# Kernel optimization log

Measured on AMD Instinct MI355X. Metric: run time of the kernel, lower is better.

## Reference

```python
import jax, jax.numpy as jnp
import numpy as np

B, T, L, D, H = 8, 4, 512, 512, 8
HD = D // H
THR = 1.0
BETA = 0.5
EPS = 1e-5


def heaviside(x):
    return (x >= 0).astype(x.dtype)


def bn_eval(x, g, b, rm, rv):
    # BatchNorm1d in eval mode applied on the last dim
    return (x - rm) * (g * jax.lax.rsqrt(rv + EPS)) + b


def lif(x_btld):
    # snntorch Leaky(beta=0.5, threshold=1, reset='subtract'), mem init 0, scan over T
    xs = jnp.moveaxis(x_btld, 1, 0)  # (T,B,L,D)

    def step(mem, xt):
        reset = heaviside(mem - THR)          # reset from previous mem (detached in torch)
        mem = BETA * mem + xt - reset * THR
        spk = heaviside(mem - THR)
        return mem, spk

    _, spks = jax.lax.scan(step, jnp.zeros_like(xs[0]), xs)
    return jnp.moveaxis(spks, 0, 1)


def setup_inputs() -> dict:
    key = jax.random.key(0)
    ks = jax.random.split(key, 24)
    s = D ** -0.5
    inp = {
        "x": jax.random.normal(ks[0], (B, T, L, D), jnp.float32),
        "q_w": jax.random.normal(ks[1], (D, D), jnp.float32) * s,
        "q_g": jax.random.normal(ks[2], (D,), jnp.float32),
        "q_b": jax.random.normal(ks[3], (D,), jnp.float32),
        "q_rm": jax.random.normal(ks[4], (D,), jnp.float32),
        "q_rv": jax.random.uniform(ks[5], (D,), jnp.float32),
        "k_w": jax.random.normal(ks[6], (D, D), jnp.float32) * s,
        "k_g": jax.random.normal(ks[7], (D,), jnp.float32),
        "k_b": jax.random.normal(ks[8], (D,), jnp.float32),
        "k_rm": jax.random.normal(ks[9], (D,), jnp.float32),
        "k_rv": jax.random.uniform(ks[10], (D,), jnp.float32),
        "v_w": jax.random.normal(ks[11], (D, D), jnp.float32) * s,
        "v_g": jax.random.normal(ks[12], (D,), jnp.float32),
        "v_b": jax.random.normal(ks[13], (D,), jnp.float32),
        "v_rm": jax.random.normal(ks[14], (D,), jnp.float32),
        "v_rv": jax.random.uniform(ks[15], (D,), jnp.float32),
        "o_w": jax.random.normal(ks[16], (D, D), jnp.float32) * s,
        "o_bias": jax.random.normal(ks[17], (D,), jnp.float32),
        "o_g": jax.random.normal(ks[18], (D,), jnp.float32),
        "o_b": jax.random.normal(ks[19], (D,), jnp.float32),
        "o_rm": jax.random.normal(ks[20], (D,), jnp.float32),
        "o_rv": jax.random.uniform(ks[21], (D,), jnp.float32),
    }
    return inp


def reference(x, q_w, q_g, q_b, q_rm, q_rv, k_w, k_g, k_b, k_rm, k_rv,
              v_w, v_g, v_b, v_rm, v_rv, o_w, o_bias, o_g, o_b, o_rm, o_rv):
    scale = HD ** -0.5
    # Q path: linear -> BN -> LIF (binary {0,1})
    q = bn_eval(jnp.einsum('btld,ed->btle', x, q_w), q_g, q_b, q_rm, q_rv)
    q = lif(q)
    # K path: linear -> BN -> ReLU (continuous)
    k = jax.nn.relu(bn_eval(jnp.einsum('btld,ed->btle', x, k_w), k_g, k_b, k_rm, k_rv))
    # V path: linear -> BN -> ternary {-1,0,+1}
    v = bn_eval(jnp.einsum('btld,ed->btle', x, v_w), v_g, v_b, v_rm, v_rv)
    v = heaviside(v - THR) - heaviside(-v - THR)
    # split heads: (B,T,H,L,hd)
    sh = lambda a: a.reshape(B, T, L, H, HD).transpose(0, 1, 3, 2, 4)
    q, k, v = sh(q), sh(k), sh(v)
    attn = jnp.einsum('bthld,bthmd->bthlm', q, k) * scale
    out = jnp.einsum('bthlm,bthmd->bthld', attn, v)
    out = out.transpose(0, 1, 3, 2, 4).reshape(B, T, L, D)
    out = jnp.einsum('btld,ed->btle', out, o_w) + o_bias
    out = bn_eval(out, o_g, o_b, o_rm, o_rv)
    return lif(out)
```

## Files before the change

kernel.cpp:

```cpp
#include <hip/hip_runtime.h>
#include <math.h>
#include <stdint.h>

#define Bb 8
#define Tt 4
#define Ll 512
#define Dd 512
#define Hh 8
#define HDd 64
#define Mm (Bb*Tt*Ll)

typedef _Float16 f16;
typedef _Float16 f16x8 __attribute__((ext_vector_type(8)));
typedef _Float16 f16x4 __attribute__((ext_vector_type(4)));
typedef float f32x16 __attribute__((ext_vector_type(16)));

#define LO_SCALE 2048.0f
#define LO_INV   4.8828125e-4f

__device__ __forceinline__ void gload16(const void* g, void* l) {
  __builtin_amdgcn_global_load_lds(
      (const __attribute__((address_space(1))) unsigned int*)(uintptr_t)g,
      (__attribute__((address_space(3))) unsigned int*)(uintptr_t)l,
      16, 0, 0);
}

struct SplitArgs {
  const float* src[5];
  f16* hi[5];
  f16* lo[5];
};

__global__ void split_k(SplitArgs s) {
  int i = blockIdx.x * 256 + threadIdx.x;
  int seg, base;
  if (i < 1048576) { seg = 0; base = i; }
  else { int r = i - 1048576; seg = 1 + (r >> 15); base = r & 32767; }
  const float* sp = s.src[seg] + (size_t)base * 8;
  float4 v0 = *(const float4*)sp;
  float4 v1 = *(const float4*)(sp + 4);
  float a[8] = {v0.x, v0.y, v0.z, v0.w, v1.x, v1.y, v1.z, v1.w};
  f16x8 hv, lv;
  #pragma unroll
  for (int e = 0; e < 8; ++e) {
    f16 hh = (f16)a[e];
    hv[e] = hh;
    lv[e] = (f16)((a[e] - (float)hh) * LO_SCALE);
  }
  *(f16x8*)(s.hi[seg] + (size_t)base * 8) = hv;
  *(f16x8*)(s.lo[seg] + (size_t)base * 8) = lv;
}

struct GArgs {
  const f16 *Ah, *Al;
  const f16 *Wh0, *Wl0, *Wh1, *Wl1, *Wh2, *Wl2;
  const float *g0,*b0,*rm0,*rv0;
  const float *g1,*b1,*rm1,*rv1;
  const float *g2,*b2,*rm2,*rv2;
  const float* bias;
  f16*   oq;
  float* ok;
  f16*   ov;
  float* oo;
};

#define SMEM_BYTES 34048

template<int MODE>
__global__ __launch_bounds__(256, 2)
void gemm_f16(GArgs ar) {
  extern __shared__ __align__(16) char smem[];
  f16* Ah_s = (f16*)smem;
  f16* Al_s = (f16*)(smem + 8192);
  f16* Bh_s = (f16*)(smem + 16384);
  f16* Bl_s = (f16*)(smem + 24576);
  float (*TS)[133] = (float(*)[133])smem;

  const int tid = threadIdx.x;
  const int lane = tid & 63, wid = tid >> 6;

  const int bid = blockIdx.x;
  int bx, by;
  if (MODE == 0) { const int sw = (bid & 7) * 192 + (bid >> 3); bx = sw % 12; by = sw / 12; }
  else           { const int sw = (bid & 7) * 64  + (bid >> 3); bx = sw & 3;  by = sw >> 2; }

  const int seg = (MODE == 0) ? (bx >> 2) : 0;
  const int lc0 = (MODE == 0) ? ((bx & 3) << 7) : (bx << 7);
  const int b = by >> 4, lc32 = by & 15;

  const f16* Wh = (seg == 0 ? ar.Wh0 : (seg == 1 ? ar.Wh1 : ar.Wh2));
  const f16* Wl = (seg == 0 ? ar.Wl0 : (seg == 1 ? ar.Wl1 : ar.Wl2));
  const float* gp  = (seg == 0 ? ar.g0  : (seg == 1 ? ar.g1  : ar.g2));
  const float* bp  = (seg == 0 ? ar.b0  : (seg == 1 ? ar.b1  : ar.b2));
  const float* rmp = (seg == 0 ? ar.rm0 : (seg == 1 ? ar.rm1 : ar.rm2));
  const float* rvp = (seg == 0 ? ar.rv0 : (seg == 1 ? ar.rv1 : ar.rv2));

  const int sr = lane >> 2, skc = lane & 3;
  const int skcs = skc ^ ((sr >> 1) & 3);
  const int frow = lane & 31, khalf = lane >> 5;
  const int rsw = (frow >> 1) & 3;
  const int wmr = wid >> 1, wnc = wid & 1;

  f32x16 acc_h[2][2], acc_l[2][2];
  #pragma unroll
  for (int i = 0; i < 2; ++i)
    #pragma unroll
    for (int j = 0; j < 2; ++j) {
      acc_h[i][j] = (f32x16)0.0f;
      acc_l[i][j] = (f32x16)0.0f;
    }

  for (int k0 = 0; k0 < Dd; k0 += 32) {
    __syncthreads();
    #pragma unroll
    for (int i = 0; i < 2; ++i) {
      const int r = i * 64 + wid * 16 + sr;
      const int growA = (((b << 2) + (r >> 5)) << 9) + (lc32 << 5) + (r & 31);
      const size_t goA = (size_t)growA * Dd + k0 + skcs * 8;
      const size_t goB = (size_t)(lc0 + r) * Dd + k0 + skcs * 8;
      const int lb = i * 2048 + wid * 512;
      gload16(ar.Ah + goA, Ah_s + lb);
      gload16(ar.Al + goA, Al_s + lb);
      gload16(Wh + goB, Bh_s + lb);
      gload16(Wl + goB, Bl_s + lb);
    }
    __syncthreads();

    f16x8 ah[2][2], al[2][2], bh[2][2], bl[2][2];
    #pragma unroll
    for (int mi = 0; mi < 2; ++mi) {
      const int r = wmr * 64 + mi * 32 + frow;
      #pragma unroll
      for (int ks = 0; ks < 2; ++ks) {
        const int cin = (khalf + 2 * ks) ^ rsw;
        const int ad = r * 32 + cin * 8;
        ah[mi][ks] = *(const f16x8*)&Ah_s[ad];
        al[mi][ks] = *(const f16x8*)&Al_s[ad];
      }
    }
    #pragma unroll
    for (int nj = 0; nj < 2; ++nj) {
      const int r = wnc * 64 + nj * 32 + frow;
      #pragma unroll
      for (int ks = 0; ks < 2; ++ks) {
        const int cin = (khalf + 2 * ks) ^ rsw;
        const int ad = r * 32 + cin * 8;
        bh[nj][ks] = *(const f16x8*)&Bh_s[ad];
        bl[nj][ks] = *(const f16x8*)&Bl_s[ad];
      }
    }
    #pragma unroll
    for (int ks = 0; ks < 2; ++ks)
      #pragma unroll
      for (int mi = 0; mi < 2; ++mi)
        #pragma unroll
        for (int nj = 0; nj < 2; ++nj) {
          acc_h[mi][nj] = __builtin_amdgcn_mfma_f32_32x32x16_f16(ah[mi][ks], bh[nj][ks], acc_h[mi][nj], 0, 0, 0);
          acc_l[mi][nj] = __builtin_amdgcn_mfma_f32_32x32x16_f16(ah[mi][ks], bl[nj][ks], acc_l[mi][nj], 0, 0, 0);
          acc_l[mi][nj] = __builtin_amdgcn_mfma_f32_32x32x16_f16(al[mi][ks], bh[nj][ks], acc_l[mi][nj], 0, 0, 0);
        }
  }

  float scl[2], shc[2];
  #pragma unroll
  for (int nj = 0; nj < 2; ++nj) {
    const int c = lc0 + wnc * 64 + nj * 32 + frow;
    double S = (double)gp[c] / sqrt((double)rvp[c] + 1e-5);
    double Sh = (double)bp[c] - (double)rmp[c] * S;
    if (MODE == 1) Sh += (double)ar.bias[c] * S;
    scl[nj] = (float)S; shc[nj] = (float)Sh;
  }

  if (MODE == 0 && seg != 0) {
    #pragma unroll
    for (int mi = 0; mi < 2; ++mi)
      #pragma unroll
      for (int nj = 0; nj < 2; ++nj)
        #pragma unroll
        for (int r = 0; r < 16; ++r) {
          const int row32 = (r & 3) + 8 * (r >> 2) + 4 * khalf;
          const int tr = wmr * 64 + mi * 32 + row32;
          const int grow = (((b << 2) + (tr >> 5)) << 9) + (lc32 << 5) + (tr & 31);
          const int col = lc0 + wnc * 64 + nj * 32 + frow;
          float val = acc_h[mi][nj][r] + acc_l[mi][nj][r] * LO_INV;
          float y = val * scl[nj] + shc[nj];
          if (seg == 1) ar.ok[(size_t)grow * Dd + col] = fmaxf(y, 0.f);
          else ar.ov[(size_t)grow * Dd + col] =
                   (f16)((y >= 1.f ? 1.f : 0.f) - (-y >= 1.f ? 1.f : 0.f));
        }
    return;
  }

  __syncthreads();
  #pragma unroll
  for (int half = 0; half < 2; ++half) {
    if (wnc == half) {
      #pragma unroll
      for (int mi = 0; mi < 2; ++mi)
        #pragma unroll
        for (int nj = 0; nj < 2; ++nj)
          #pragma unroll
          for (int q = 0; q < 4; ++q) {
            float4 yv;
            float* yp = &yv.x;
            #pragma unroll
            for (int rr = 0; rr < 4; ++rr) {
              const int r = q * 4 + rr;
              float val = acc_h[mi][nj][r] + acc_l[mi][nj][r] * LO_INV;
              yp[rr] = val * scl[nj] + shc[nj];
            }
            *(float4*)&TS[nj * 32 + frow][wmr * 64 + mi * 32 + 8 * q + 4 * khalf] = yv;
          }
    }
    __syncthreads();
    const int cc4 = (tid & 15) << 2;
    #pragma unroll
    for (int rr = 0; rr < 2; ++rr) {
      const int rl = (tid >> 4) + (rr << 4);
      float mm[4] = {0.f, 0.f, 0.f, 0.f};
      #pragma unroll
      for (int t = 0; t < 4; ++t) {
        const int trow = t * 32 + rl;
        float sp[4];
        #pragma unroll
        for (int c = 0; c < 4; ++c) {
          float y = TS[cc4 + c][trow];
          float rst = (mm[c] >= 1.f) ? 1.f : 0.f;
          mm[c] = 0.5f * mm[c] + y - rst;
          sp[c] = (mm[c] >= 1.f) ? 1.f : 0.f;
        }
        const size_t go = ((size_t)((((b << 2) + t) << 9) + (lc32 << 5) + rl)) * Dd
                          + lc0 + (half << 6) + cc4;
        if (MODE == 0) {
          f16x4 s4;
          s4[0] = (f16)sp[0]; s4[1] = (f16)sp[1]; s4[2] = (f16)sp[2]; s4[3] = (f16)sp[3];
          *(f16x4*)(ar.oq + go) = s4;
        } else {
          *(float4*)(ar.oo + go) = make_float4(sp[0], sp[1], sp[2], sp[3]);
        }
      }
    }
    __syncthreads();
  }
}

__global__ __launch_bounds__(256)
void attn_g(const float* __restrict__ ks, const f16* __restrict__ vs,
            float* __restrict__ pG) {
  const int bt = blockIdx.x, h = blockIdx.y, c = blockIdx.z;
  const float* kp = ks + (size_t)bt * Ll * Dd + h * HDd;
  const f16* vp = vs + (size_t)bt * Ll * Dd + h * HDd;

  __shared__ float KS[64][68];
  __shared__ float VS[64][68];
  const int tid = threadIdx.x;
  const int te = tid & 15, td = tid >> 4;

  float gacc[4][4];
  #pragma unroll
  for (int i = 0; i < 4; ++i)
    #pragma unroll
    for (int j = 0; j < 4; ++j) gacc[i][j] = 0.f;

  for (int mt = 0; mt < 2; ++mt) {
    const int m0 = c * 128 + mt * 64;
    #pragma unroll
    for (int it = 0; it < 4; ++it) {
      int fidx = it * 256 + tid;
      int row = fidx >> 4, fq = fidx & 15;
      *(float4*)&KS[row][fq << 2] = *(const float4*)(kp + (size_t)(m0 + row) * Dd + (fq << 2));
    }
    #pragma unroll
    for (int it = 0; it < 2; ++it) {
      int fidx = it * 256 + tid;
      int row = fidx >> 3, c8 = fidx & 7;
      f16x8 hv = *(const f16x8*)(vp + (size_t)(m0 + row) * Dd + (c8 << 3));
      *(float4*)&VS[row][c8 << 3] = make_float4(hv[0], hv[1], hv[2], hv[3]);
      *(float4*)&VS[row][(c8 << 3) + 4] = make_float4(hv[4], hv[5], hv[6], hv[7]);
    }
    __syncthreads();
    #pragma unroll 4
    for (int mm = 0; mm < 64; ++mm) {
      float4 k4 = *(const float4*)&KS[mm][te << 2];
      float4 v4 = *(const float4*)&VS[mm][td << 2];
      const float kk[4] = {k4.x, k4.y, k4.z, k4.w};
      const float vv[4] = {v4.x, v4.y, v4.z, v4.w};
      #pragma unroll
      for (int i = 0; i < 4; ++i)
        #pragma unroll
        for (int j = 0; j < 4; ++j)
          gacc[i][j] = fmaf(kk[i], vv[j], gacc[i][j]);
    }
    __syncthreads();
  }
  float* out = pG + (((size_t)(bt * 8 + h) * 4 + c) << 12);
  #pragma unroll
  for (int i = 0; i < 4; ++i)
    *(float4*)&out[((te << 2) + i) * 64 + (td << 2)] =
        make_float4(gacc[i][0] * 0.125f, gacc[i][1] * 0.125f,
                    gacc[i][2] * 0.125f, gacc[i][3] * 0.125f);
}

__global__ __launch_bounds__(256)
void attn_o(const f16* __restrict__ qs, const float* __restrict__ pG,
            f16* __restrict__ ahi, f16* __restrict__ alo) {
  const int bt = blockIdx.x, h = blockIdx.y, lc = blockIdx.z;
  __shared__ float G[64][68];
  __shared__ float QS[64][68];
  const int tid = threadIdx.x;

  const float* pg = pG + (((size_t)(bt * 8 + h) * 4) << 12);
  #pragma unroll
  for (int rep = 0; rep < 4; ++rep) {
    int t4 = rep * 256 + tid;
    int e = t4 >> 4, dq = t4 & 15;
    int off = e * 64 + (dq << 2);
    float4 s0 = *(const float4*)(pg + off);
    float4 s1 = *(const float4*)(pg + 4096 + off);
    float4 s2 = *(const float4*)(pg + 8192 + off);
    float4 s3 = *(const float4*)(pg + 12288 + off);
    *(float4*)&G[e][dq << 2] = make_float4(s0.x + s1.x + s2.x + s3.x,
                                           s0.y + s1.y + s2.y + s3.y,
                                           s0.z + s1.z + s2.z + s3.z,
                                           s0.w + s1.w + s2.w + s3.w);
  }
  __syncthreads();

  const f16* qp = qs + (size_t)bt * Ll * Dd + h * HDd;
  const int lr = tid >> 2, dg = tid & 3;

  for (int l0 = 0; l0 < 128; l0 += 64) {
    #pragma unroll
    for (int it = 0; it < 2; ++it) {
      int fidx = it * 256 + tid;
      int row = fidx >> 3, c8 = fidx & 7;
      f16x8 hv = *(const f16x8*)(qp + (size_t)(lc * 128 + l0 + row) * Dd + (c8 << 3));
      *(float4*)&QS[row][c8 << 3] = make_float4(hv[0], hv[1], hv[2], hv[3]);
      *(float4*)&QS[row][(c8 << 3) + 4] = make_float4(hv[4], hv[5], hv[6], hv[7]);
    }
    __syncthreads();
    float oacc[16];
    #pragma unroll
    for (int j = 0; j < 16; ++j) oacc[j] = 0.f;
    for (int ee = 0; ee < 64; ++ee) {
      float qv = QS[lr][ee];
      #pragma unroll
      for (int jq = 0; jq < 4; ++jq) {
        float4 g4 = *(const float4*)&G[ee][(dg << 4) + (jq << 2)];
        oacc[jq * 4 + 0] = fmaf(qv, g4.x, oacc[jq * 4 + 0]);
        oacc[jq * 4 + 1] = fmaf(qv, g4.y, oacc[jq * 4 + 1]);
        oacc[jq * 4 + 2] = fmaf(qv, g4.z, oacc[jq * 4 + 2]);
        oacc[jq * 4 + 3] = fmaf(qv, g4.w, oacc[jq * 4 + 3]);
      }
    }
    f16x8 h0, l0v, h1, l1v;
    #pragma unroll
    for (int t = 0; t < 8; ++t) {
      float v = oacc[t];
      f16 hh = (f16)v;
      h0[t] = hh; l0v[t] = (f16)((v - (float)hh) * LO_SCALE);
      float v2 = oacc[8 + t];
      f16 hh2 = (f16)v2;
      h1[t] = hh2; l1v[t] = (f16)((v2 - (float)hh2) * LO_SCALE);
    }
    size_t ob = ((size_t)bt * Ll + lc * 128 + l0 + lr) * Dd + h * HDd + (dg << 4);
    *(f16x8*)(ahi + ob) = h0;
    *(f16x8*)(ahi + ob + 8) = h1;
    *(f16x8*)(alo + ob) = l0v;
    *(f16x8*)(alo + ob + 8) = l1v;
    __syncthreads();
  }
}

extern "C" void kernel_launch(void* const* d_in, const int* in_sizes, int n_in,
                              void* d_out, int out_size, void* d_ws, size_t ws_size,
                              hipStream_t stream) {
  const float* x    = (const float*)d_in[0];
  const float* q_w  = (const float*)d_in[1];
  const float* q_g  = (const float*)d_in[2];
  const float* q_b  = (const float*)d_in[3];
  const float* q_rm = (const float*)d_in[4];
  const float* q_rv = (const float*)d_in[5];
  const float* k_w  = (const float*)d_in[6];
  const float* k_g  = (const float*)d_in[7];
  const float* k_b  = (const float*)d_in[8];
  const float* k_rm = (const float*)d_in[9];
  const float* k_rv = (const float*)d_in[10];
  const float* v_w  = (const float*)d_in[11];
  const float* v_g  = (const float*)d_in[12];
  const float* v_b  = (const float*)d_in[13];
  const float* v_rm = (const float*)d_in[14];
  const float* v_rv = (const float*)d_in[15];
  const float* o_w  = (const float*)d_in[16];
  const float* o_bias = (const float*)d_in[17];
  const float* o_g  = (const float*)d_in[18];
  const float* o_b  = (const float*)d_in[19];
  const float* o_rm = (const float*)d_in[20];
  const float* o_rv = (const float*)d_in[21];

  char* wsb = (char*)d_ws;
  const size_t R16 = 16777216;
  f16*   xhi  = (f16*)wsb;
  f16*   xlo  = (f16*)(wsb + R16);
  f16*   qspk = (f16*)(wsb + 2 * R16);
  float* kbuf = (float*)(wsb + 3 * R16);
  f16*   vbuf = (f16*)(wsb + 5 * R16);
  float* pG   = (float*)(wsb + 6 * R16);
  f16*   wsp  = (f16*)(wsb + 7 * R16);
  f16* qwh = wsp;            f16* qwl = wsp + 262144;
  f16* kwh = wsp + 2*262144; f16* kwl = wsp + 3*262144;
  f16* vwh = wsp + 4*262144; f16* vwl = wsp + 5*262144;
  f16* owh = wsp + 6*262144; f16* owl = wsp + 7*262144;
  f16* ahi = xhi;
  f16* alo = xlo;

  SplitArgs sa;
  sa.src[0] = x;   sa.hi[0] = xhi; sa.lo[0] = xlo;
  sa.src[1] = q_w; sa.hi[1] = qwh; sa.lo[1] = qwl;
  sa.src[2] = k_w; sa.hi[2] = kwh; sa.lo[2] = kwl;
  sa.src[3] = v_w; sa.hi[3] = vwh; sa.lo[3] = vwl;
  sa.src[4] = o_w; sa.hi[4] = owh; sa.lo[4] = owl;
  split_k<<<4608, 256, 0, stream>>>(sa);

  GArgs a1;
  a1.Ah = xhi; a1.Al = xlo;
  a1.Wh0 = qwh; a1.Wl0 = qwl; a1.Wh1 = kwh; a1.Wl1 = kwl; a1.Wh2 = vwh; a1.Wl2 = vwl;
  a1.g0 = q_g; a1.b0 = q_b; a1.rm0 = q_rm; a1.rv0 = q_rv;
  a1.g1 = k_g; a1.b1 = k_b; a1.rm1 = k_rm; a1.rv1 = k_rv;
  a1.g2 = v_g; a1.b2 = v_b; a1.rm2 = v_rm; a1.rv2 = v_rv;
  a1.bias = nullptr;
  a1.oq = qspk; a1.ok = kbuf; a1.ov = vbuf; a1.oo = nullptr;
  gemm_f16<0><<<1536, 256, SMEM_BYTES, stream>>>(a1);

  attn_g<<<dim3(32, 8, 4), 256, 0, stream>>>(kbuf, vbuf, pG);
  attn_o<<<dim3(32, 8, 4), 256, 0, stream>>>(qspk, pG, ahi, alo);

  GArgs a2;
  a2.Ah = ahi; a2.Al = alo;
  a2.Wh0 = owh; a2.Wl0 = owl; a2.Wh1 = owh; a2.Wl1 = owl; a2.Wh2 = owh; a2.Wl2 = owl;
  a2.g0 = o_g; a2.b0 = o_b; a2.rm0 = o_rm; a2.rv0 = o_rv;
  a2.g1 = o_g; a2.b1 = o_b; a2.rm1 = o_rm; a2.rv1 = o_rv;
  a2.g2 = o_g; a2.b2 = o_b; a2.rm2 = o_rm; a2.rv2 = o_rv;
  a2.bias = o_bias;
  a2.oq = nullptr; a2.ok = nullptr; a2.ov = nullptr; a2.oo = (float*)d_out;
  gemm_f16<1><<<512, 256, SMEM_BYTES, stream>>>(a2);
}
```

Baseline: 297.0 us.

## Fuse fp16 hi/lo split into GEMM tile loads and merge attention kernels

Removes the standalone split kernel. The GEMMs now load fp32 A and W tiles into shared memory with a swizzle and convert them to fp16 hi/lo pairs in registers using packed round-toward-zero conversion. The two attention kernels (partial K^T V, then Q·G) are merged into one kernel per (bt, head), and it writes fp32 output that the final GEMM consumes directly. This removes the extra global round trips for the split buffers and the partial-G reduction. In exchange, each tile is converted repeatedly by every block that reads it, the fused attention grid has a quarter as many blocks, and rounding behaviour changes because RTZ replaces round-to-nearest.

Measured after the change: 331.2 us. 1.11x slower.

```diff
diff --git a/kernel.cpp b/kernel.cpp
--- a/kernel.cpp
+++ b/kernel.cpp
@@ -13,6 +13,7 @@
 typedef _Float16 f16;
 typedef _Float16 f16x8 __attribute__((ext_vector_type(8)));
 typedef _Float16 f16x4 __attribute__((ext_vector_type(4)));
+typedef float f32x4 __attribute__((ext_vector_type(4)));
 typedef float f32x16 __attribute__((ext_vector_type(16)));
 
 #define LO_SCALE 2048.0f
@@ -25,35 +26,21 @@
       16, 0, 0);
 }
 
-struct SplitArgs {
-  const float* src[5];
-  f16* hi[5];
-  f16* lo[5];
-};
-
-__global__ void split_k(SplitArgs s) {
-  int i = blockIdx.x * 256 + threadIdx.x;
-  int seg, base;
-  if (i < 1048576) { seg = 0; base = i; }
-  else { int r = i - 1048576; seg = 1 + (r >> 15); base = r & 32767; }
-  const float* sp = s.src[seg] + (size_t)base * 8;
-  float4 v0 = *(const float4*)sp;
-  float4 v1 = *(const float4*)(sp + 4);
-  float a[8] = {v0.x, v0.y, v0.z, v0.w, v1.x, v1.y, v1.z, v1.w};
-  f16x8 hv, lv;
-  #pragma unroll
-  for (int e = 0; e < 8; ++e) {
-    f16 hh = (f16)a[e];
-    hv[e] = hh;
-    lv[e] = (f16)((a[e] - (float)hh) * LO_SCALE);
-  }
-  *(f16x8*)(s.hi[seg] + (size_t)base * 8) = hv;
-  *(f16x8*)(s.lo[seg] + (size_t)base * 8) = lv;
+__device__ __forceinline__ void cvt_split8(f32x4 u0, f32x4 u1, f16x8& hi, f16x8& lo) {
+  float s[8] = {u0[0], u0[1], u0[2], u0[3], u1[0], u1[1], u1[2], u1[3]};
+  #pragma unroll
+  for (int e = 0; e < 8; e += 2) {
+    auto h = __builtin_amdgcn_cvt_pkrtz(s[e], s[e + 1]);
+    auto l = __builtin_amdgcn_cvt_pkrtz((s[e] - (float)h[0]) * LO_SCALE,
+                                        (s[e + 1] - (float)h[1]) * LO_SCALE);
+    hi[e] = h[0]; hi[e + 1] = h[1];
+    lo[e] = l[0]; lo[e + 1] = l[1];
+  }
 }
 
 struct GArgs {
-  const f16 *Ah, *Al;
-  const f16 *Wh0, *Wl0, *Wh1, *Wl1, *Wh2, *Wl2;
+  const float* A;
+  const float *W0, *W1, *W2;
   const float *g0,*b0,*rm0,*rv0;
   const float *g1,*b1,*rm1,*rv1;
   const float *g2,*b2,*rm2,*rv2;
@@ -70,10 +57,8 @@
 __global__ __launch_bounds__(256, 2)
 void gemm_f16(GArgs ar) {
   extern __shared__ __align__(16) char smem[];
-  f16* Ah_s = (f16*)smem;
-  f16* Al_s = (f16*)(smem + 8192);
-  f16* Bh_s = (f16*)(smem + 16384);
-  f16* Bl_s = (f16*)(smem + 24576);
+  float* As = (float*)smem;
+  float* Bs = (float*)(smem + 16384);
   float (*TS)[133] = (float(*)[133])smem;
 
   const int tid = threadIdx.x;
@@ -88,17 +73,14 @@
   const int lc0 = (MODE == 0) ? ((bx & 3) << 7) : (bx << 7);
   const int b = by >> 4, lc32 = by & 15;
 
-  const f16* Wh = (seg == 0 ? ar.Wh0 : (seg == 1 ? ar.Wh1 : ar.Wh2));
-  const f16* Wl = (seg == 0 ? ar.Wl0 : (seg == 1 ? ar.Wl1 : ar.Wl2));
+  const float* Wsel = (MODE == 0) ? (seg == 0 ? ar.W0 : (seg == 1 ? ar.W1 : ar.W2)) : ar.W0;
   const float* gp  = (seg == 0 ? ar.g0  : (seg == 1 ? ar.g1  : ar.g2));
   const float* bp  = (seg == 0 ? ar.b0  : (seg == 1 ? ar.b1  : ar.b2));
   const float* rmp = (seg == 0 ? ar.rm0 : (seg == 1 ? ar.rm1 : ar.rm2));
   const float* rvp = (seg == 0 ? ar.rv0 : (seg == 1 ? ar.rv1 : ar.rv2));
 
-  const int sr = lane >> 2, skc = lane & 3;
-  const int skcs = skc ^ ((sr >> 1) & 3);
+  const int srow8 = tid >> 3, sch = tid & 7;
   const int frow = lane & 31, khalf = lane >> 5;
-  const int rsw = (frow >> 1) & 3;
   const int wmr = wid >> 1, wnc = wid & 1;
 
   f32x16 acc_h[2][2], acc_l[2][2];
@@ -113,16 +95,13 @@
   for (int k0 = 0; k0 < Dd; k0 += 32) {
     __syncthreads();
     #pragma unroll
-    for (int i = 0; i < 2; ++i) {
-      const int r = i * 64 + wid * 16 + sr;
+    for (int j = 0; j < 4; ++j) {
+      const int r = j * 32 + srow8;
+      const int g = sch ^ (r & 7);
       const int growA = (((b << 2) + (r >> 5)) << 9) + (lc32 << 5) + (r & 31);
-      const size_t goA = (size_t)growA * Dd + k0 + skcs * 8;
-      const size_t goB = (size_t)(lc0 + r) * Dd + k0 + skcs * 8;
-      const int lb = i * 2048 + wid * 512;
-      gload16(ar.Ah + goA, Ah_s + lb);
-      gload16(ar.Al + goA, Al_s + lb);
-      gload16(Wh + goB, Bh_s + lb);
-      gload16(Wl + goB, Bl_s + lb);
+      const int lb = (j * 32 + (wid << 3)) << 5;
+      gload16(ar.A + (size_t)growA * Dd + k0 + g * 4, As + lb);
+      gload16(Wsel + (size_t)(lc0 + r) * Dd + k0 + g * 4, Bs + lb);
     }
     __syncthreads();
 
@@ -132,10 +111,11 @@
       const int r = wmr * 64 + mi * 32 + frow;
       #pragma unroll
       for (int ks = 0; ks < 2; ++ks) {
-        const int cin = (khalf + 2 * ks) ^ rsw;
-        const int ad = r * 32 + cin * 8;
-        ah[mi][ks] = *(const f16x8*)&Ah_s[ad];
-        al[mi][ks] = *(const f16x8*)&Al_s[ad];
+        const int c0 = 4 * ks + 2 * khalf;
+        const int p0 = c0 ^ (r & 7), p1 = (c0 + 1) ^ (r & 7);
+        f32x4 u0 = *(const f32x4*)&As[r * 32 + p0 * 4];
+        f32x4 u1 = *(const f32x4*)&As[r * 32 + p1 * 4];
+        cvt_split8(u0, u1, ah[mi][ks], al[mi][ks]);
       }
     }
     #pragma unroll
@@ -143,10 +123,11 @@
       const int r = wnc * 64 + nj * 32 + frow;
       #pragma unroll
       for (int ks = 0; ks < 2; ++ks) {
-        const int cin = (khalf + 2 * ks) ^ rsw;
-        const int ad = r * 32 + cin * 8;
-        bh[nj][ks] = *(const f16x8*)&Bh_s[ad];
-        bl[nj][ks] = *(const f16x8*)&Bl_s[ad];
+        const int c0 = 4 * ks + 2 * khalf;
+        const int p0 = c0 ^ (r & 7), p1 = (c0 + 1) ^ (r & 7);
+        f32x4 u0 = *(const f32x4*)&Bs[r * 32 + p0 * 4];
+        f32x4 u1 = *(const f32x4*)&Bs[r * 32 + p1 * 4];
+        cvt_split8(u0, u1, bh[nj][ks], bl[nj][ks]);
       }
     }
     #pragma unroll
@@ -245,14 +226,18 @@
 }
 
 __global__ __launch_bounds__(256)
-void attn_g(const float* __restrict__ ks, const f16* __restrict__ vs,
-            float* __restrict__ pG) {
-  const int bt = blockIdx.x, h = blockIdx.y, c = blockIdx.z;
+void attn_f(const f16* __restrict__ qs, const float* __restrict__ ks,
+            const f16* __restrict__ vs, float* __restrict__ outp) {
+  const int bt = blockIdx.x, h = blockIdx.y;
   const float* kp = ks + (size_t)bt * Ll * Dd + h * HDd;
   const f16* vp = vs + (size_t)bt * Ll * Dd + h * HDd;
+  const f16* qp = qs + (size_t)bt * Ll * Dd + h * HDd;
+  float* op = outp + (size_t)bt * Ll * Dd + h * HDd;
 
   __shared__ float KS[64][68];
   __shared__ float VS[64][68];
+  __shared__ float G[64][68];
+
   const int tid = threadIdx.x;
   const int te = tid & 15, td = tid >> 4;
 
@@ -262,8 +247,7 @@
     #pragma unroll
     for (int j = 0; j < 4; ++j) gacc[i][j] = 0.f;
 
-  for (int mt = 0; mt < 2; ++mt) {
-    const int m0 = c * 128 + mt * 64;
+  for (int m0 = 0; m0 < Ll; m0 += 64) {
     #pragma unroll
     for (int it = 0; it < 4; ++it) {
       int fidx = it * 256 + tid;
@@ -293,57 +277,29 @@
     }
     __syncthreads();
   }
-  float* out = pG + (((size_t)(bt * 8 + h) * 4 + c) << 12);
   #pragma unroll
   for (int i = 0; i < 4; ++i)
-    *(float4*)&out[((te << 2) + i) * 64 + (td << 2)] =
+    *(float4*)&G[(te << 2) + i][td << 2] =
         make_float4(gacc[i][0] * 0.125f, gacc[i][1] * 0.125f,
                     gacc[i][2] * 0.125f, gacc[i][3] * 0.125f);
-}
-
-__global__ __launch_bounds__(256)
-void attn_o(const f16* __restrict__ qs, const float* __restrict__ pG,
-            f16* __restrict__ ahi, f16* __restrict__ alo) {
-  const int bt = blockIdx.x, h = blockIdx.y, lc = blockIdx.z;
-  __shared__ float G[64][68];
-  __shared__ float QS[64][68];
-  const int tid = threadIdx.x;
-
-  const float* pg = pG + (((size_t)(bt * 8 + h) * 4) << 12);
-  #pragma unroll
-  for (int rep = 0; rep < 4; ++rep) {
-    int t4 = rep * 256 + tid;
-    int e = t4 >> 4, dq = t4 & 15;
-    int off = e * 64 + (dq << 2);
-    float4 s0 = *(const float4*)(pg + off);
-    float4 s1 = *(const float4*)(pg + 4096 + off);
-    float4 s2 = *(const float4*)(pg + 8192 + off);
-    float4 s3 = *(const float4*)(pg + 12288 + off);
-    *(float4*)&G[e][dq << 2] = make_float4(s0.x + s1.x + s2.x + s3.x,
-                                           s0.y + s1.y + s2.y + s3.y,
-                                           s0.z + s1.z + s2.z + s3.z,
-                                           s0.w + s1.w + s2.w + s3.w);
-  }
   __syncthreads();
 
-  const f16* qp = qs + (size_t)bt * Ll * Dd + h * HDd;
   const int lr = tid >> 2, dg = tid & 3;
-
-  for (int l0 = 0; l0 < 128; l0 += 64) {
+  for (int l0 = 0; l0 < Ll; l0 += 64) {
     #pragma unroll
     for (int it = 0; it < 2; ++it) {
       int fidx = it * 256 + tid;
       int row = fidx >> 3, c8 = fidx & 7;
-      f16x8 hv = *(const f16x8*)(qp + (size_t)(lc * 128 + l0 + row) * Dd + (c8 << 3));
-      *(float4*)&QS[row][c8 << 3] = make_float4(hv[0], hv[1], hv[2], hv[3]);
-      *(float4*)&QS[row][(c8 << 3) + 4] = make_float4(hv[4], hv[5], hv[6], hv[7]);
+      f16x8 hv = *(const f16x8*)(qp + (size_t)(l0 + row) * Dd + (c8 << 3));
+      *(float4*)&KS[row][c8 << 3] = make_float4(hv[0], hv[1], hv[2], hv[3]);
+      *(float4*)&KS[row][(c8 << 3) + 4] = make_float4(hv[4], hv[5], hv[6], hv[7]);
     }
     __syncthreads();
     float oacc[16];
     #pragma unroll
     for (int j = 0; j < 16; ++j) oacc[j] = 0.f;
     for (int ee = 0; ee < 64; ++ee) {
-      float qv = QS[lr][ee];
+      float qv = KS[lr][ee];
       #pragma unroll
       for (int jq = 0; jq < 4; ++jq) {
         float4 g4 = *(const float4*)&G[ee][(dg << 4) + (jq << 2)];
@@ -353,21 +309,11 @@
         oacc[jq * 4 + 3] = fmaf(qv, g4.w, oacc[jq * 4 + 3]);
       }
     }
-    f16x8 h0, l0v, h1, l1v;
-    #pragma unroll
-    for (int t = 0; t < 8; ++t) {
-      float v = oacc[t];
-      f16 hh = (f16)v;
-      h0[t] = hh; l0v[t] = (f16)((v - (float)hh) * LO_SCALE);
-      float v2 = oacc[8 + t];
-      f16 hh2 = (f16)v2;
-      h1[t] = hh2; l1v[t] = (f16)((v2 - (float)hh2) * LO_SCALE);
-    }
-    size_t ob = ((size_t)bt * Ll + lc * 128 + l0 + lr) * Dd + h * HDd + (dg << 4);
-    *(f16x8*)(ahi + ob) = h0;
-    *(f16x8*)(ahi + ob + 8) = h1;
-    *(f16x8*)(alo + ob) = l0v;
-    *(f16x8*)(alo + ob + 8) = l1v;
+    #pragma unroll
+    for (int jq = 0; jq < 4; ++jq)
+      *(float4*)(op + (size_t)(l0 + lr) * Dd + (dg << 4) + (jq << 2)) =
+          make_float4(oacc[jq * 4 + 0], oacc[jq * 4 + 1],
+                      oacc[jq * 4 + 2], oacc[jq * 4 + 3]);
     __syncthreads();
   }
 }
@@ -400,31 +346,14 @@
 
   char* wsb = (char*)d_ws;
   const size_t R16 = 16777216;
-  f16*   xhi  = (f16*)wsb;
-  f16*   xlo  = (f16*)(wsb + R16);
-  f16*   qspk = (f16*)(wsb + 2 * R16);
-  float* kbuf = (float*)(wsb + 3 * R16);
-  f16*   vbuf = (f16*)(wsb + 5 * R16);
-  float* pG   = (float*)(wsb + 6 * R16);
-  f16*   wsp  = (f16*)(wsb + 7 * R16);
-  f16* qwh = wsp;            f16* qwl = wsp + 262144;
-  f16* kwh = wsp + 2*262144; f16* kwl = wsp + 3*262144;
-  f16* vwh = wsp + 4*262144; f16* vwl = wsp + 5*262144;
-  f16* owh = wsp + 6*262144; f16* owl = wsp + 7*262144;
-  f16* ahi = xhi;
-  f16* alo = xlo;
-
-  SplitArgs sa;
-  sa.src[0] = x;   sa.hi[0] = xhi; sa.lo[0] = xlo;
-  sa.src[1] = q_w; sa.hi[1] = qwh; sa.lo[1] = qwl;
-  sa.src[2] = k_w; sa.hi[2] = kwh; sa.lo[2] = kwl;
-  sa.src[3] = v_w; sa.hi[3] = vwh; sa.lo[3] = vwl;
-  sa.src[4] = o_w; sa.hi[4] = owh; sa.lo[4] = owl;
-  split_k<<<4608, 256, 0, stream>>>(sa);
+  f16*   qspk = (f16*)wsb;
+  float* kbuf = (float*)(wsb + R16);
+  f16*   vbuf = (f16*)(wsb + 3 * R16);
+  float* abuf = (float*)(wsb + 4 * R16);
 
   GArgs a1;
-  a1.Ah = xhi; a1.Al = xlo;
-  a1.Wh0 = qwh; a1.Wl0 = qwl; a1.Wh1 = kwh; a1.Wl1 = kwl; a1.Wh2 = vwh; a1.Wl2 = vwl;
+  a1.A = x;
+  a1.W0 = q_w; a1.W1 = k_w; a1.W2 = v_w;
   a1.g0 = q_g; a1.b0 = q_b; a1.rm0 = q_rm; a1.rv0 = q_rv;
   a1.g1 = k_g; a1.b1 = k_b; a1.rm1 = k_rm; a1.rv1 = k_rv;
   a1.g2 = v_g; a1.b2 = v_b; a1.rm2 = v_rm; a1.rv2 = v_rv;
@@ -432,12 +361,11 @@
   a1.oq = qspk; a1.ok = kbuf; a1.ov = vbuf; a1.oo = nullptr;
   gemm_f16<0><<<1536, 256, SMEM_BYTES, stream>>>(a1);
 
-  attn_g<<<dim3(32, 8, 4), 256, 0, stream>>>(kbuf, vbuf, pG);
-  attn_o<<<dim3(32, 8, 4), 256, 0, stream>>>(qspk, pG, ahi, alo);
+  attn_f<<<dim3(32, 8), 256, 0, stream>>>(qspk, kbuf, vbuf, abuf);
 
   GArgs a2;
-  a2.Ah = ahi; a2.Al = alo;
-  a2.Wh0 = owh; a2.Wl0 = owl; a2.Wh1 = owh; a2.Wl1 = owl; a2.Wh2 = owh; a2.Wl2 = owl;
+  a2.A = abuf;
+  a2.W0 = o_w; a2.W1 = o_w; a2.W2 = o_w;
   a2.g0 = o_g; a2.b0 = o_b; a2.rm0 = o_rm; a2.rv0 = o_rv;
   a2.g1 = o_g; a2.b1 = o_b; a2.rm1 = o_rm; a2.rv1 = o_rv;
   a2.g2 = o_g; a2.b2 = o_b; a2.rm2 = o_rm; a2.rv2 = o_rv;
```
